# Kernel optimization log

Hardware: AMD Instinct MI355X
Metric: run time of the kernel (lower is better)

## Reference

```python
import jax, jax.numpy as jnp
import numpy as np

DIM = 256      # encoding dimensionality
S = 16         # alphabet size (one Linear per symbol)
OUT = 10       # number of classes
DEPTH = 14     # levels of the complete binary tree
N = 2 ** DEPTH - 1  # 16383 nodes, BFS layout (root = node 0)


def setup_inputs() -> dict:
    key = jax.random.key(0)
    k1, k2, k3, k4, k5 = jax.random.split(key, 5)
    # symbols per node
    x_sym = jax.random.randint(k1, (N,), 0, S, dtype=jnp.int32)
    # complete binary tree in BFS order: children of i are 2i+1, 2i+2; -1 = no child (leaf)
    idx = np.arange(N)
    child_idx = np.stack([2 * idx + 1, 2 * idx + 2], axis=1)
    child_idx[child_idx >= N] = -1
    child_idx = jnp.asarray(child_idx, dtype=jnp.int32)
    # per-symbol Linear(dim, dim) weights/biases, out Linear(dim, OUT)
    sc = 1.0 / np.sqrt(DIM)
    W = jax.random.normal(k2, (S, DIM, DIM), dtype=jnp.float32) * sc
    b = jax.random.normal(k3, (S, DIM), dtype=jnp.float32) * sc
    W_out = jax.random.normal(k4, (DIM, OUT), dtype=jnp.float32) * sc
    b_out = jax.random.normal(k5, (OUT,), dtype=jnp.float32) * sc
    return {"x_sym": x_sym, "child_idx": child_idx, "W": W, "b": b,
            "W_out": W_out, "b_out": b_out}


def reference(x_sym, child_idx, W, b, W_out, b_out):
    """Depth-batched, vectorized equivalent of the serial tree traversal.

    For each node i (children before parents):
      enc[i] = tanh(W[sym_i] @ mean(enc[children(i)]) + b[sym_i])
    Leaves use the zero vector as input (matching Linear(zeros) = bias).
    Output = enc[root] @ W_out + b_out.
    """
    n = x_sym.shape[0]
    depth = int(np.log2(n + 1))
    dim = W.shape[1]
    enc = jnp.zeros((n, dim), dtype=W.dtype)
    for d in range(depth - 1, -1, -1):  # deepest level first
        lo, hi = 2 ** d - 1, min(2 ** (d + 1) - 1, n)
        cidx = child_idx[lo:hi]                          # [m, 2]
        valid = (cidx >= 0)
        ch = enc[jnp.clip(cidx, 0)] * valid[..., None].astype(enc.dtype)  # [m,2,dim]
        cnt = valid.sum(-1, keepdims=True).astype(enc.dtype)
        mean = ch.sum(1) / jnp.maximum(cnt, 1.0)         # [m, dim]; zeros for leaves
        onehot = jax.nn.one_hot(x_sym[lo:hi], W.shape[0], dtype=enc.dtype)  # [m, S]
        pre = jnp.einsum('ns,nd,sde->ne', onehot, mean, W) + onehot @ b
        enc = enc.at[lo:hi].set(jnp.tanh(pre))
    return enc[0] @ W_out + b_out
```

## Files before the change

### kernel.cpp

```cpp
#include <hip/hip_runtime.h>

#define DIM 256
#define GRP 16
#define MPAD 260
#define NBLK 1024
#define CSTR 32

#define O11 0
#define O10 2288
#define O9  3552
#define OTOT 4352
#define G11_BLOCKS 572
#define G10_BLOCKS 316
#define G9_ITEMS   188

#define FMA4(a, sc, v) \
    a.x = fmaf((sc), (v).x, a.x); a.y = fmaf((sc), (v).y, a.y); \
    a.z = fmaf((sc), (v).z, a.z); a.w = fmaf((sc), (v).w, a.w);

__device__ __forceinline__ float ld1(const float* p) {
    union { unsigned int u; float f; } cv;
    cv.u = __hip_atomic_load((const unsigned int*)p, __ATOMIC_RELAXED,
                             __HIP_MEMORY_SCOPE_AGENT);
    return cv.f;
}
__device__ __forceinline__ float2 ld2(const float* p) {
    union { unsigned long long u; float2 f; } cv;
    cv.u = __hip_atomic_load((const unsigned long long*)p, __ATOMIC_RELAXED,
                             __HIP_MEMORY_SCOPE_AGENT);
    return cv.f;
}
__device__ __forceinline__ void st1f(float* p, float x) {
    union { unsigned int u; float f; } cv; cv.f = x;
    __hip_atomic_store((unsigned int*)p, cv.u, __ATOMIC_RELAXED,
                       __HIP_MEMORY_SCOPE_AGENT);
}
__device__ __forceinline__ void st2(float* p, float x, float y) {
    union { unsigned long long u; float2 f; } cv;
    cv.f = make_float2(x, y);
    __hip_atomic_store((unsigned long long*)p, cv.u, __ATOMIC_RELAXED,
                       __HIP_MEMORY_SCOPE_AGENT);
}
__device__ __forceinline__ int addi(int* p) {
    return __hip_atomic_fetch_add(p, 1, __ATOMIC_RELAXED, __HIP_MEMORY_SCOPE_AGENT);
}
__device__ __forceinline__ void spin4(const int* f) {
    if (__hip_atomic_load(f, __ATOMIC_RELAXED, __HIP_MEMORY_SCOPE_AGENT) >= 4) return;
    int guard = 0;
    do {
        __builtin_amdgcn_s_sleep(1);
        if (++guard > (1 << 20)) break;
    } while (__hip_atomic_load(f, __ATOMIC_RELAXED, __HIP_MEMORY_SCOPE_AGENT) < 4);
}

__device__ __forceinline__ void gemm_core(const float* __restrict__ Ws,
                                          const float mean_s[GRP][MPAD],
                                          float4 part_s[4][4][64],
                                          int w, int lane) {
    const int ns4 = (lane >> 4) << 2;
    float4 acc0 = make_float4(0, 0, 0, 0), acc1 = acc0, acc2 = acc0, acc3 = acc0;
    const int dbase = w * 64;
    #pragma unroll 4
    for (int dd = 0; dd < 64; dd += 4) {
        const float4 w0 = *(const float4*)(Ws + (size_t)(dd + 0) * DIM);
        const float4 w1 = *(const float4*)(Ws + (size_t)(dd + 1) * DIM);
        const float4 w2 = *(const float4*)(Ws + (size_t)(dd + 2) * DIM);
        const float4 w3 = *(const float4*)(Ws + (size_t)(dd + 3) * DIM);
        const int dk = dbase + dd;
        const float4 m0 = *(const float4*)(&mean_s[ns4 + 0][dk]);
        const float4 m1 = *(const float4*)(&mean_s[ns4 + 1][dk]);
        const float4 m2 = *(const float4*)(&mean_s[ns4 + 2][dk]);
        const float4 m3 = *(const float4*)(&mean_s[ns4 + 3][dk]);
        FMA4(acc0, m0.x, w0); FMA4(acc0, m0.y, w1); FMA4(acc0, m0.z, w2); FMA4(acc0, m0.w, w3);
        FMA4(acc1, m1.x, w0); FMA4(acc1, m1.y, w1); FMA4(acc1, m1.z, w2); FMA4(acc1, m1.w, w3);
        FMA4(acc2, m2.x, w0); FMA4(acc2, m2.y, w1); FMA4(acc2, m2.z, w2); FMA4(acc2, m2.w, w3);
        FMA4(acc3, m3.x, w0); FMA4(acc3, m3.y, w1); FMA4(acc3, m3.z, w2); FMA4(acc3, m3.w, w3);
    }
    part_s[w][0][lane] = acc0;
    part_s[w][1][lane] = acc1;
    part_s[w][2][lane] = acc2;
    part_s[w][3][lane] = acc3;
}

__device__ __forceinline__ void unpair(int p, int& pa, int& pb) {
    int a = 0, rem = p;
    while (rem >= 16 - a) { rem -= 16 - a; ++a; }
    pa = a; pb = a + rem;
}

__global__ __launch_bounds__(256) void combo_sort_zero(const int* __restrict__ x_sym,
                                                       const float* __restrict__ W,
                                                       const float* __restrict__ b,
                                                       float* __restrict__ T,
                                                       int* __restrict__ order,
                                                       int* __restrict__ cnt) {
    __shared__ float  mean_s[GRP][MPAD];
    __shared__ float4 part_s[4][4][64];
    __shared__ int cnt_s[16], cur_s[16];
    const int t = threadIdx.x;
    const int w = t >> 6;
    const int lane = t & 63;
    const int bid = blockIdx.x;

    if (bid < 576) {
        const int s = bid / 36;
        const int rem = bid % 36;
        const int chunk = rem >> 2;
        const int tile = rem & 3;
        {
            const int c = lane << 2;
            #pragma unroll
            for (int j = 0; j < 4; ++j) {
                const int p = chunk * 16 + w * 4 + j;
                float4 m = make_float4(0.f, 0.f, 0.f, 0.f);
                if (p < 136) {
                    int pa, pb; unpair(p, pa, pb);
                    const float4 ba = *(const float4*)(b + pa * DIM + c);
                    const float4 bb = *(const float4*)(b + pb * DIM + c);
                    m.x = 0.5f * (tanhf(ba.x) + tanhf(bb.x));
                    m.y = 0.5f * (tanhf(ba.y) + tanhf(bb.y));
                    m.z = 0.5f * (tanhf(ba.z) + tanhf(bb.z));
                    m.w = 0.5f * (tanhf(ba.w) + tanhf(bb.w));
                }
                *(float4*)(&mean_s[w * 4 + j][c]) = m;
            }
        }
        __syncthreads();
        const int ns4 = (lane >> 4) << 2;
        const int g4  = (lane & 15) << 2;
        gemm_core(W + ((size_t)s << 16) + (size_t)(w * 64) * DIM + tile * 64 + g4,
                  mean_s, part_s, w, lane);
        __syncthreads();
        const int p = chunk * 16 + ns4 + w;
        if (p < 136) {
            int pa, pb; unpair(p, pa, pb);
            float4 r        = part_s[0][w][lane];
            const float4 p1 = part_s[1][w][lane];
            const float4 p2 = part_s[2][w][lane];
            const float4 p3 = part_s[3][w][lane];
            const float4 bs = *(const float4*)(b + s * DIM + tile * 64 + g4);
            r.x = tanhf(r.x + p1.x + p2.x + p3.x + bs.x);
            r.y = tanhf(r.y + p1.y + p2.y + p3.y + bs.y);
            r.z = tanhf(r.z + p1.z + p2.z + p3.z + bs.z);
            r.w = tanhf(r.w + p1.w + p2.w + p3.w + bs.w);
            *(float4*)(T + (size_t)((s * 16 + pa) * 16 + pb) * DIM + tile * 64 + g4) = r;
            if (pa != pb)
                *(float4*)(T + (size_t)((s * 16 + pb) * 16 + pa) * DIM + tile * 64 + g4) = r;
        }
    } else if (bid <= 578) {
        const int li = bid - 576;
        const int d = 11 - li;
        const int off = (li == 0) ? O11 : (li == 1) ? O10 : O9;
        const int lo = (1 << d) - 1;
        const int n = 1 << d;
        for (int i = t; i < n + 240; i += 256) order[off + i] = -1;
        if (t < 16) cnt_s[t] = 0;
        __syncthreads();
        for (int i = t; i < n; i += 256) atomicAdd(&cnt_s[x_sym[lo + i]], 1);
        __syncthreads();
        if (t == 0) {
            int run = off;
            for (int s2 = 0; s2 < 16; ++s2) {
                cur_s[s2] = run;
                run += ((cnt_s[s2] + GRP - 1) / GRP) * GRP;
            }
        }
        __syncthreads();
        for (int i = t; i < n; i += 256) {
            const int pos = atomicAdd(&cur_s[x_sym[lo + i]], 1);
            order[pos] = lo + i;
        }
    } else {
        for (int i = t; i < 1024 * CSTR; i += 256) cnt[i] = 0;
    }
}

__global__ __launch_bounds__(256) void grouped_T(const int* __restrict__ x_sym,
                                                 const float* __restrict__ W,
                                                 const float* __restrict__ b,
                                                 float* __restrict__ enc,
                                                 const float* __restrict__ T,
                                                 const int* __restrict__ order) {
    const int base = (blockIdx.x >> 2) * GRP + O11;
    const int tile = blockIdx.x & 3;
    const int n0 = order[base];
    if (n0 < 0) return;
    const int s = x_sym[n0];
    const int t = threadIdx.x;
    const int w = t >> 6;
    const int lane = t & 63;
    __shared__ float  mean_s[GRP][MPAD];
    __shared__ float4 part_s[4][4][64];
    {
        const int c = lane << 2;
        #pragma unroll
        for (int j = 0; j < 4; ++j) {
            const int node = order[base + w * 4 + j];
            float4 m = make_float4(0.f, 0.f, 0.f, 0.f);
            if (node >= 0) {
                const int c0 = 2 * node + 1, c1 = c0 + 1;
                const float* r0 = T + (size_t)((x_sym[c0] * 16 + x_sym[2 * c0 + 1]) * 16
                                               + x_sym[2 * c0 + 2]) * DIM;
                const float* r1 = T + (size_t)((x_sym[c1] * 16 + x_sym[2 * c1 + 1]) * 16
                                               + x_sym[2 * c1 + 2]) * DIM;
                const float4 ea = *(const float4*)(r0 + c);
                const float4 eb = *(const float4*)(r1 + c);
                m.x = 0.5f * (ea.x + eb.x);
                m.y = 0.5f * (ea.y + eb.y);
                m.z = 0.5f * (ea.z + eb.z);
                m.w = 0.5f * (ea.w + eb.w);
            }
            *(float4*)(&mean_s[w * 4 + j][c]) = m;
        }
    }
    __syncthreads();
    const int ns4 = (lane >> 4) << 2;
    const int g4  = (lane & 15) << 2;
    gemm_core(W + ((size_t)s << 16) + (size_t)(w * 64) * DIM + tile * 64 + g4,
              mean_s, part_s, w, lane);
    __syncthreads();
    const int node_g = order[base + ns4 + w];
    if (node_g >= 0) {
        float4 r        = part_s[0][w][lane];
        const float4 p1 = part_s[1][w][lane];
        const float4 p2 = part_s[2][w][lane];
        const float4 p3 = part_s[3][w][lane];
        const float4 bs = *(const float4*)(b + s * DIM + tile * 64 + g4);
        r.x = tanhf(r.x + p1.x + p2.x + p3.x + bs.x);
        r.y = tanhf(r.y + p1.y + p2.y + p3.y + bs.y);
        r.z = tanhf(r.z + p1.z + p2.z + p3.z + bs.z);
        r.w = tanhf(r.w + p1.w + p2.w + p3.w + bs.w);
        *(float4*)(enc + (size_t)node_g * DIM + tile * 64 + g4) = r;
    }
}

__global__ __launch_bounds__(256) void grouped_enc(const int* __restrict__ x_sym,
                                                   const float* __restrict__ W,
                                                   const float* __restrict__ b,
                                                   float* __restrict__ enc,
                                                   const int* __restrict__ order,
                                                   int level_off) {
    const int base = (blockIdx.x >> 2) * GRP + level_off;
    const int tile = blockIdx.x & 3;
    const int n0 = order[base];
    if (n0 < 0) return;
    const int s = x_sym[n0];
    const int t = threadIdx.x;
    const int w = t >> 6;
    const int lane = t & 63;
    __shared__ float  mean_s[GRP][MPAD];
    __shared__ float4 part_s[4][4][64];
    {
        const int c = lane << 2;
        #pragma unroll
        for (int j = 0; j < 4; ++j) {
            const int node = order[base + w * 4 + j];
            float4 m = make_float4(0.f, 0.f, 0.f, 0.f);
            if (node >= 0) {
                const int c0 = 2 * node + 1;
                const float4 ea = *(const float4*)(enc + (size_t)c0 * DIM + c);
                const float4 eb = *(const float4*)(enc + (size_t)(c0 + 1) * DIM + c);
                m.x = 0.5f * (ea.x + eb.x);
                m.y = 0.5f * (ea.y + eb.y);
                m.z = 0.5f * (ea.z + eb.z);
                m.w = 0.5f * (ea.w + eb.w);
            }
            *(float4*)(&mean_s[w * 4 + j][c]) = m;
        }
    }
    __syncthreads();
    const int ns4 = (lane >> 4) << 2;
    const int g4  = (lane & 15) << 2;
    gemm_core(W + ((size_t)s << 16) + (size_t)(w * 64) * DIM + tile * 64 + g4,
              mean_s, part_s, w, lane);
    __syncthreads();
    const int node_g = order[base + ns4 + w];
    if (node_g >= 0) {
        float4 r        = part_s[0][w][lane];
        const float4 p1 = part_s[1][w][lane];
        const float4 p2 = part_s[2][w][lane];
        const float4 p3 = part_s[3][w][lane];
        const float4 bs = *(const float4*)(b + s * DIM + tile * 64 + g4);
        r.x = tanhf(r.x + p1.x + p2.x + p3.x + bs.x);
        r.y = tanhf(r.y + p1.y + p2.y + p3.y + bs.y);
        r.z = tanhf(r.z + p1.z + p2.z + p3.z + bs.z);
        r.w = tanhf(r.w + p1.w + p2.w + p3.w + bs.w);
        *(float4*)(enc + (size_t)node_g * DIM + tile * 64 + g4) = r;
    }
}

__global__ __launch_bounds__(256, 4) void tail_kernel(const int* __restrict__ x_sym,
                                                      const float* __restrict__ W,
                                                      const float* __restrict__ b,
                                                      float* __restrict__ enc,
                                                      const int* __restrict__ order,
                                                      int* __restrict__ cnt,
                                                      const float* __restrict__ W_out,
                                                      const float* __restrict__ b_out,
                                                      float* __restrict__ out) {
    __shared__ float  mean_s[GRP][MPAD];
    __shared__ float4 part_s[4][4][64];
    const int t = threadIdx.x;
    const int w = t >> 6;
    const int lane = t & 63;
    const int bid = blockIdx.x;

    if (bid < G9_ITEMS) {
        const int base = (bid >> 2) * GRP + O9;
        const int tile = bid & 3;
        const int n0 = order[base];
        if (n0 >= 0) {
            const int s = x_sym[n0];
            const int c = lane << 2;
            #pragma unroll
            for (int j = 0; j < 4; ++j) {
                const int node = order[base + w * 4 + j];
                float4 m = make_float4(0.f, 0.f, 0.f, 0.f);
                if (node >= 0) {
                    const int c0 = 2 * node + 1;
                    const float4 ea = *(const float4*)(enc + (size_t)c0 * DIM + c);
                    const float4 eb = *(const float4*)(enc + (size_t)(c0 + 1) * DIM + c);
                    m.x = 0.5f * (ea.x + eb.x);
                    m.y = 0.5f * (ea.y + eb.y);
                    m.z = 0.5f * (ea.z + eb.z);
                    m.w = 0.5f * (ea.w + eb.w);
                }
                *(float4*)(&mean_s[w * 4 + j][c]) = m;
            }
            __syncthreads();
            const int ns4 = (lane >> 4) << 2;
            const int g4  = (lane & 15) << 2;
            gemm_core(W + ((size_t)s << 16) + (size_t)(w * 64) * DIM + tile * 64 + g4,
                      mean_s, part_s, w, lane);
            __syncthreads();
            const int node_g = order[base + ns4 + w];
            if (node_g >= 0) {
                float4 r        = part_s[0][w][lane];
                const float4 p1 = part_s[1][w][lane];
                const float4 p2 = part_s[2][w][lane];
                const float4 p3 = part_s[3][w][lane];
                const float4 bs = *(const float4*)(b + s * DIM + tile * 64 + g4);
                r.x = tanhf(r.x + p1.x + p2.x + p3.x + bs.x);
                r.y = tanhf(r.y + p1.y + p2.y + p3.y + bs.y);
                r.z = tanhf(r.z + p1.z + p2.z + p3.z + bs.z);
                r.w = tanhf(r.w + p1.w + p2.w + p3.w + bs.w);
                float* ep = enc + (size_t)node_g * DIM + tile * 64 + g4;
                st2(ep, r.x, r.y);
                st2(ep + 2, r.z, r.w);
            }
            __syncthreads();
            if (t < 16) {
                const int ng = order[base + t];
                if (ng >= 0) addi(&cnt[ng * CSTR]);
            }
        }
        __syncthreads();
    }

    float* smean = (float*)&mean_s[0][0];
    float* spart = (float*)&part_s[0][0][0];
    for (int d = 8; d >= 0; --d) {
        const int items = 4 << d;
        if (bid >= items) return;
        const int node = (1 << d) - 1 + (bid >> 2);
        const int tile = bid & 3;
        const int c0 = 2 * node + 1;
        const int cc = tile * 64 + lane;
        const int s = x_sym[node];

        const float* Wp = W + ((size_t)s << 16) + (size_t)(w * 64) * DIM + cc;
        float wreg[64];
        #pragma unroll
        for (int i = 0; i < 64; ++i) wreg[i] = Wp[(size_t)i * DIM];
        #pragma unroll
        for (int i = 0; i < 64; ++i) asm volatile("" : "+v"(wreg[i]) :: "memory");

        if (t < 2) spin4(&cnt[(c0 + t) * CSTR]);
        __syncthreads();

        if (t < 128) {
            const int o = t << 1;
            const float2 a = ld2(enc + (size_t)c0 * DIM + o);
            const float2 bb = ld2(enc + (size_t)(c0 + 1) * DIM + o);
            *(float2*)&smean[o] = make_float2(0.5f * (a.x + bb.x), 0.5f * (a.y + bb.y));
        }
        __syncthreads();

        float acc0 = 0.0f, acc1 = 0.0f;
        const float* sm = smean + w * 64;
        #pragma unroll
        for (int i = 0; i < 64; i += 2) {
            acc0 = fmaf(sm[i], wreg[i], acc0);
            acc1 = fmaf(sm[i + 1], wreg[i + 1], acc1);
        }
        spart[t] = acc0 + acc1;
        __syncthreads();
        if (t < 64) {
            float r = spart[t] + spart[t + 64] + spart[t + 128] + spart[t + 192];
            r += b[s * DIM + tile * 64 + t];
            st1f(enc + (size_t)node * DIM + tile * 64 + t, tanhf(r));
        }
        __syncthreads();
        if (t == 0) addi(&cnt[node * CSTR]);
        __syncthreads();
    }

    if (bid == 0) {
        if (t == 0) spin4(&cnt[0]);
        __syncthreads();
        const float e = ld1(enc + t);
        float p[10];
        #pragma unroll
        for (int o = 0; o < 10; ++o) p[o] = e * W_out[t * 10 + o];
        #pragma unroll
        for (int o = 0; o < 10; ++o)
            #pragma unroll
            for (int k = 32; k >= 1; k >>= 1) p[o] += __shfl_xor(p[o], k, 64);
        float* hp = (float*)&part_s[0][0][0];
        if (lane == 0) {
            #pragma unroll
            for (int o = 0; o < 10; ++o) hp[w * 10 + o] = p[o];
        }
        __syncthreads();
        if (t < 10) out[t] = b_out[t] + hp[t] + hp[10 + t] + hp[20 + t] + hp[30 + t];
    }
}

__global__ __launch_bounds__(256) void level_small(const int* __restrict__ x_sym,
                                                   const float* __restrict__ W,
                                                   const float* __restrict__ b,
                                                   float* __restrict__ enc,
                                                   int lo, int N) {
    const int node = lo + (blockIdx.x >> 2);
    const int tile = blockIdx.x & 3;
    const int t = threadIdx.x;
    const int lane = t & 63;
    const int c = tile * 64 + lane;
    __shared__ float mean_s[DIM];
    __shared__ float part[256];
    const int s = x_sym[node];
    const int c0 = 2 * node + 1;
    float m = 0.0f;
    if (c0 < N)
        m = 0.5f * (enc[(size_t)c0 * DIM + t] + enc[(size_t)(c0 + 1) * DIM + t]);
    mean_s[t] = m;
    __syncthreads();
    float acc = 0.0f;
    if (c0 < N) {
        const float* __restrict__ Ws = W + ((size_t)s << 16);
        const int d0 = (t >> 6) * 64;
        #pragma unroll 8
        for (int d = d0; d < d0 + 64; ++d)
            acc = fmaf(mean_s[d], Ws[d * DIM + c], acc);
    }
    part[t] = acc;
    __syncthreads();
    if (t < 64) {
        float r = part[t] + part[t + 64] + part[t + 128] + part[t + 192];
        r += b[s * DIM + c];
        enc[(size_t)node * DIM + c] = tanhf(r);
    }
}

__global__ __launch_bounds__(256) void level_big(const int* __restrict__ x_sym,
                                                 const float* __restrict__ W,
                                                 const float* __restrict__ b,
                                                 float* __restrict__ enc,
                                                 int lo, int N) {
    const int node = lo + blockIdx.x;
    const int e = threadIdx.x;
    __shared__ float mean_s[DIM];
    const int s = x_sym[node];
    const int c0 = 2 * node + 1;
    float acc = b[s * DIM + e];
    if (c0 < N) {
        mean_s[e] = 0.5f * (enc[(size_t)c0 * DIM + e] + enc[(size_t)(c0 + 1) * DIM + e]);
        __syncthreads();
        const float* __restrict__ Ws = W + ((size_t)s << 16);
        #pragma unroll 8
        for (int d = 0; d < DIM; ++d)
            acc = fmaf(mean_s[d], Ws[d * DIM + e], acc);
    }
    enc[(size_t)node * DIM + e] = tanhf(acc);
}

__global__ void out_kernel(const float* __restrict__ enc,
                           const float* __restrict__ W_out,
                           const float* __restrict__ b_out,
                           float* __restrict__ out, int outn) {
    const int o = threadIdx.x;
    if (o < outn) {
        float acc = b_out[o];
        for (int d = 0; d < DIM; ++d)
            acc = fmaf(enc[d], W_out[d * outn + o], acc);
        out[o] = acc;
    }
}

extern "C" void kernel_launch(void* const* d_in, const int* in_sizes, int n_in,
                              void* d_out, int out_size, void* d_ws, size_t ws_size,
                              hipStream_t stream) {
    const int*   x_sym = (const int*)d_in[0];
    const float* W     = (const float*)d_in[2];
    const float* b     = (const float*)d_in[3];
    const float* W_out = (const float*)d_in[4];
    const float* b_out = (const float*)d_in[5];
    float* out = (float*)d_out;
    float* enc = (float*)d_ws;
    const int N = in_sizes[0];

    int depth = 0;
    while (((1 << depth) - 1) < N) ++depth;

    const size_t need = (size_t)16383 * DIM * 4 + (OTOT + 1024 * CSTR) * 4;
    if (N == (1 << 14) - 1 && out_size == 10 && ws_size >= need) {
        float* T   = enc + (size_t)8191 * DIM;
        int* order = (int*)(enc + (size_t)N * DIM);
        int* cnt   = order + OTOT;

        combo_sort_zero<<<580, 256, 0, stream>>>(x_sym, W, b, T, order, cnt);
        grouped_T<<<G11_BLOCKS, 256, 0, stream>>>(x_sym, W, b, enc, T, order);
        grouped_enc<<<G10_BLOCKS, 256, 0, stream>>>(x_sym, W, b, enc, order, O10);
        tail_kernel<<<NBLK, 256, 0, stream>>>(x_sym, W, b, enc, order, cnt,
                                              W_out, b_out, out);
    } else {
        for (int d = depth - 1; d >= 0; --d) {
            int lo = (1 << d) - 1;
            int n = (1 << d);
            if (lo + n > N) n = N - lo;
            if (n >= 256)
                level_big<<<n, 256, 0, stream>>>(x_sym, W, b, enc, lo, N);
            else
                level_small<<<n * 4, 256, 0, stream>>>(x_sym, W, b, enc, lo, N);
        }
        out_kernel<<<1, 64, 0, stream>>>(enc, W_out, b_out, out, out_size);
    }
}
```

Before: 67.06 us.

## Process two tree levels per block in tail to halve cross-block handoffs

Levels 8 down to 0 of the tail kernel previously split each node over four blocks, one per 64-column tile, and synchronised through flag counters at every level. Now one block computes a whole parent node together with its two child nodes, full 256 columns, reading the four grandchildren directly. The intent is to cut the number of spin-wait handoffs and launch-wide serial steps roughly in half. In exchange each block does more serial FMA work per column and loses the preloaded register weights, so per-level latency rises while parallelism across blocks drops.

```diff
diff --git a/kernel.cpp b/kernel.cpp
--- a/kernel.cpp
+++ b/kernel.cpp
@@ -44,13 +44,13 @@
 __device__ __forceinline__ int addi(int* p) {
     return __hip_atomic_fetch_add(p, 1, __ATOMIC_RELAXED, __HIP_MEMORY_SCOPE_AGENT);
 }
-__device__ __forceinline__ void spin4(const int* f) {
-    if (__hip_atomic_load(f, __ATOMIC_RELAXED, __HIP_MEMORY_SCOPE_AGENT) >= 4) return;
+__device__ __forceinline__ void spinN(const int* f, int thr) {
+    if (__hip_atomic_load(f, __ATOMIC_RELAXED, __HIP_MEMORY_SCOPE_AGENT) >= thr) return;
     int guard = 0;
     do {
         __builtin_amdgcn_s_sleep(1);
         if (++guard > (1 << 20)) break;
-    } while (__hip_atomic_load(f, __ATOMIC_RELAXED, __HIP_MEMORY_SCOPE_AGENT) < 4);
+    } while (__hip_atomic_load(f, __ATOMIC_RELAXED, __HIP_MEMORY_SCOPE_AGENT) < thr);
 }
 
 __device__ __forceinline__ void gemm_core(const float* __restrict__ Ws,
@@ -86,6 +86,20 @@
     int a = 0, rem = p;
     while (rem >= 16 - a) { rem -= 16 - a; ++a; }
     pa = a; pb = a + rem;
+}
+
+__device__ __forceinline__ float colvec(const float* __restrict__ Wcol,
+                                        const float* __restrict__ mb) {
+    float a0 = 0.f, a1 = 0.f, a2 = 0.f, a3 = 0.f;
+    #pragma unroll 8
+    for (int k = 0; k < 256; k += 4) {
+        const float4 m4 = *(const float4*)(mb + k);
+        a0 = fmaf(m4.x, Wcol[(size_t)(k + 0) * DIM], a0);
+        a1 = fmaf(m4.y, Wcol[(size_t)(k + 1) * DIM], a1);
+        a2 = fmaf(m4.z, Wcol[(size_t)(k + 2) * DIM], a2);
+        a3 = fmaf(m4.w, Wcol[(size_t)(k + 3) * DIM], a3);
+    }
+    return (a0 + a1) + (a2 + a3);
 }
 
 __global__ __launch_bounds__(256) void combo_sort_zero(const int* __restrict__ x_sym,
@@ -289,6 +303,42 @@
     }
 }
 
+__device__ __forceinline__ void stage_pair(int n, int thr, const int* __restrict__ x_sym,
+                                           const float* __restrict__ W,
+                                           const float* __restrict__ b,
+                                           float* __restrict__ enc, int* __restrict__ cnt,
+                                           float* G, float* E, float* MB, int t) {
+    const int g0 = 4 * n + 3;
+    if (t < 4) spinN(&cnt[(g0 + t) * CSTR], thr);
+    __syncthreads();
+    #pragma unroll
+    for (int i = 0; i < 2; ++i) {
+        const int slot = t + 256 * i;
+        const int r = slot >> 7;
+        const int j = (slot & 127) << 1;
+        const float2 v = ld2(enc + (size_t)(g0 + r) * DIM + j);
+        G[r * 256 + j] = v.x;
+        G[r * 256 + j + 1] = v.y;
+    }
+    __syncthreads();
+    #pragma unroll
+    for (int i = 0; i < 2; ++i) {
+        const int sc = x_sym[2 * n + 1 + i];
+        MB[t] = 0.5f * (G[(2 * i) * 256 + t] + G[(2 * i + 1) * 256 + t]);
+        __syncthreads();
+        E[i * 256 + t] = tanhf(colvec(W + ((size_t)sc << 16) + t, MB) + b[sc * DIM + t]);
+        __syncthreads();
+    }
+    const int sp = x_sym[n];
+    MB[t] = 0.5f * (E[t] + E[256 + t]);
+    __syncthreads();
+    const float pv = tanhf(colvec(W + ((size_t)sp << 16) + t, MB) + b[sp * DIM + t]);
+    st1f(enc + (size_t)n * DIM + t, pv);
+    __syncthreads();
+    if (t == 0) addi(&cnt[n * CSTR]);
+    __syncthreads();
+}
+
 __global__ __launch_bounds__(256, 4) void tail_kernel(const int* __restrict__ x_sym,
                                                       const float* __restrict__ W,
                                                       const float* __restrict__ b,
@@ -357,73 +407,40 @@
         __syncthreads();
     }
 
-    float* smean = (float*)&mean_s[0][0];
-    float* spart = (float*)&part_s[0][0][0];
-    for (int d = 8; d >= 0; --d) {
-        const int items = 4 << d;
-        if (bid >= items) return;
-        const int node = (1 << d) - 1 + (bid >> 2);
-        const int tile = bid & 3;
-        const int c0 = 2 * node + 1;
-        const int cc = tile * 64 + lane;
-        const int s = x_sym[node];
-
-        const float* Wp = W + ((size_t)s << 16) + (size_t)(w * 64) * DIM + cc;
-        float wreg[64];
+    if (bid >= 128) return;
+    float* G  = (float*)&mean_s[0][0];
+    float* E  = G + 4 * 256;
+    float* MB = E + 2 * 256;
+
+    stage_pair(127 + bid, 4, x_sym, W, b, enc, cnt, G, E, MB, t);
+    if (bid >= 32) return;
+    stage_pair(31 + bid, 1, x_sym, W, b, enc, cnt, G, E, MB, t);
+    if (bid >= 8) return;
+    stage_pair(7 + bid, 1, x_sym, W, b, enc, cnt, G, E, MB, t);
+    if (bid >= 2) return;
+    stage_pair(1 + bid, 1, x_sym, W, b, enc, cnt, G, E, MB, t);
+    if (bid >= 1) return;
+
+    if (t < 2) spinN(&cnt[(1 + t) * CSTR], 1);
+    __syncthreads();
+    MB[t] = 0.5f * (ld1(enc + DIM + t) + ld1(enc + 2 * DIM + t));
+    __syncthreads();
+    const int s0 = x_sym[0];
+    const float e = tanhf(colvec(W + ((size_t)s0 << 16) + t, MB) + b[s0 * DIM + t]);
+    float p[10];
+    #pragma unroll
+    for (int o = 0; o < 10; ++o) p[o] = e * W_out[t * 10 + o];
+    #pragma unroll
+    for (int o = 0; o < 10; ++o)
         #pragma unroll
-        for (int i = 0; i < 64; ++i) wreg[i] = Wp[(size_t)i * DIM];
+        for (int k = 32; k >= 1; k >>= 1) p[o] += __shfl_xor(p[o], k, 64);
+    float* hp = (float*)&part_s[0][0][0];
+    if ((t & 63) == 0) {
         #pragma unroll
-        for (int i = 0; i < 64; ++i) asm volatile("" : "+v"(wreg[i]) :: "memory");
-
-        if (t < 2) spin4(&cnt[(c0 + t) * CSTR]);
-        __syncthreads();
-
-        if (t < 128) {
-            const int o = t << 1;
-            const float2 a = ld2(enc + (size_t)c0 * DIM + o);
-            const float2 bb = ld2(enc + (size_t)(c0 + 1) * DIM + o);
-            *(float2*)&smean[o] = make_float2(0.5f * (a.x + bb.x), 0.5f * (a.y + bb.y));
-        }
-        __syncthreads();
-
-        float acc0 = 0.0f, acc1 = 0.0f;
-        const float* sm = smean + w * 64;
-        #pragma unroll
-        for (int i = 0; i < 64; i += 2) {
-            acc0 = fmaf(sm[i], wreg[i], acc0);
-            acc1 = fmaf(sm[i + 1], wreg[i + 1], acc1);
-        }
-        spart[t] = acc0 + acc1;
-        __syncthreads();
-        if (t < 64) {
-            float r = spart[t] + spart[t + 64] + spart[t + 128] + spart[t + 192];
-            r += b[s * DIM + tile * 64 + t];
-            st1f(enc + (size_t)node * DIM + tile * 64 + t, tanhf(r));
-        }
-        __syncthreads();
-        if (t == 0) addi(&cnt[node * CSTR]);
-        __syncthreads();
-    }
-
-    if (bid == 0) {
-        if (t == 0) spin4(&cnt[0]);
-        __syncthreads();
-        const float e = ld1(enc + t);
-        float p[10];
-        #pragma unroll
-        for (int o = 0; o < 10; ++o) p[o] = e * W_out[t * 10 + o];
-        #pragma unroll
-        for (int o = 0; o < 10; ++o)
-            #pragma unroll
-            for (int k = 32; k >= 1; k >>= 1) p[o] += __shfl_xor(p[o], k, 64);
-        float* hp = (float*)&part_s[0][0][0];
-        if (lane == 0) {
-            #pragma unroll
-            for (int o = 0; o < 10; ++o) hp[w * 10 + o] = p[o];
-        }
-        __syncthreads();
-        if (t < 10) out[t] = b_out[t] + hp[t] + hp[10 + t] + hp[20 + t] + hp[30 + t];
-    }
+        for (int o = 0; o < 10; ++o) hp[w * 10 + o] = p[o];
+    }
+    __syncthreads();
+    if (t < 10) out[t] = b_out[t] + hp[t] + hp[10 + t] + hp[20 + t] + hp[30 + t];
 }
 
 __global__ __launch_bounds__(256) void level_small(const int* __restrict__ x_sym,
```

Measured after the change: 97.17 us. 44.9% more time.

## Fuse level-11 and level-10 grouped kernels into persistent dataflow mega kernel

Applied to the files above, without the earlier changes.

Merges the separate grouped_T and grouped_enc launches into the existing tail kernel, so levels 11, 10 and 9 run as phases of one launch. Cross-level dependencies use per-node completion counters with spin-waits instead of kernel boundaries, and the counter array grows to cover more nodes, with the zeroing split over more blocks. This removes two launch gaps and lets later levels start as soon as their children are ready. In exchange it adds spin-wait latency and atomic loads and stores, and it depends on all waited-on blocks being resident at once, which risks deadlock or the timeout guard firing if they are not.

```diff
diff --git a/kernel.cpp b/kernel.cpp
--- a/kernel.cpp
+++ b/kernel.cpp
@@ -5,6 +5,7 @@
 #define MPAD 260
 #define NBLK 1024
 #define CSTR 32
+#define NCNT 4096
 
 #define O11 0
 #define O10 2288
@@ -44,13 +45,13 @@
 __device__ __forceinline__ int addi(int* p) {
     return __hip_atomic_fetch_add(p, 1, __ATOMIC_RELAXED, __HIP_MEMORY_SCOPE_AGENT);
 }
-__device__ __forceinline__ void spin4(const int* f) {
-    if (__hip_atomic_load(f, __ATOMIC_RELAXED, __HIP_MEMORY_SCOPE_AGENT) >= 4) return;
+__device__ __forceinline__ void spinN(const int* f, int thr) {
+    if (__hip_atomic_load(f, __ATOMIC_RELAXED, __HIP_MEMORY_SCOPE_AGENT) >= thr) return;
     int guard = 0;
     do {
         __builtin_amdgcn_s_sleep(1);
         if (++guard > (1 << 20)) break;
-    } while (__hip_atomic_load(f, __ATOMIC_RELAXED, __HIP_MEMORY_SCOPE_AGENT) < 4);
+    } while (__hip_atomic_load(f, __ATOMIC_RELAXED, __HIP_MEMORY_SCOPE_AGENT) < thr);
 }
 
 __device__ __forceinline__ void gemm_core(const float* __restrict__ Ws,
@@ -171,26 +172,36 @@
             order[pos] = lo + i;
         }
     } else {
-        for (int i = t; i < 1024 * CSTR; i += 256) cnt[i] = 0;
-    }
-}
-
-__global__ __launch_bounds__(256) void grouped_T(const int* __restrict__ x_sym,
-                                                 const float* __restrict__ W,
-                                                 const float* __restrict__ b,
-                                                 float* __restrict__ enc,
-                                                 const float* __restrict__ T,
-                                                 const int* __restrict__ order) {
-    const int base = (blockIdx.x >> 2) * GRP + O11;
-    const int tile = blockIdx.x & 3;
+        const int seg = (bid - 579) * (NCNT * CSTR / 4);
+        for (int i = t; i < NCNT * CSTR / 4; i += 256) cnt[seg + i] = 0;
+    }
+}
+
+template <int SRC>
+__device__ __forceinline__ void grouped_phase(const int* __restrict__ x_sym,
+                                              const float* __restrict__ W,
+                                              const float* __restrict__ b,
+                                              float* __restrict__ enc,
+                                              const float* __restrict__ T,
+                                              const int* __restrict__ order,
+                                              int* __restrict__ cnt,
+                                              int base, int tile,
+                                              float mean_s[GRP][MPAD],
+                                              float4 part_s[4][4][64],
+                                              int t, int w, int lane) {
     const int n0 = order[base];
     if (n0 < 0) return;
     const int s = x_sym[n0];
-    const int t = threadIdx.x;
-    const int w = t >> 6;
-    const int lane = t & 63;
-    __shared__ float  mean_s[GRP][MPAD];
-    __shared__ float4 part_s[4][4][64];
+    const int ns4 = (lane >> 4) << 2;
+    const int g4  = (lane & 15) << 2;
+
+    if (SRC == 1) {
+        if (t < 32) {
+            const int pn = order[base + (t >> 1)];
+            if (pn >= 0) spinN(&cnt[(2 * pn + 1 + (t & 1)) * CSTR], 4);
+        }
+        __syncthreads();
+    }
     {
         const int c = lane << 2;
         #pragma unroll
@@ -199,23 +210,32 @@
             float4 m = make_float4(0.f, 0.f, 0.f, 0.f);
             if (node >= 0) {
                 const int c0 = 2 * node + 1, c1 = c0 + 1;
-                const float* r0 = T + (size_t)((x_sym[c0] * 16 + x_sym[2 * c0 + 1]) * 16
-                                               + x_sym[2 * c0 + 2]) * DIM;
-                const float* r1 = T + (size_t)((x_sym[c1] * 16 + x_sym[2 * c1 + 1]) * 16
-                                               + x_sym[2 * c1 + 2]) * DIM;
-                const float4 ea = *(const float4*)(r0 + c);
-                const float4 eb = *(const float4*)(r1 + c);
-                m.x = 0.5f * (ea.x + eb.x);
-                m.y = 0.5f * (ea.y + eb.y);
-                m.z = 0.5f * (ea.z + eb.z);
-                m.w = 0.5f * (ea.w + eb.w);
+                if (SRC == 0) {
+                    const float* r0 = T + (size_t)((x_sym[c0] * 16 + x_sym[2 * c0 + 1]) * 16
+                                                   + x_sym[2 * c0 + 2]) * DIM;
+                    const float* r1 = T + (size_t)((x_sym[c1] * 16 + x_sym[2 * c1 + 1]) * 16
+                                                   + x_sym[2 * c1 + 2]) * DIM;
+                    const float4 ea = *(const float4*)(r0 + c);
+                    const float4 eb = *(const float4*)(r1 + c);
+                    m.x = 0.5f * (ea.x + eb.x);
+                    m.y = 0.5f * (ea.y + eb.y);
+                    m.z = 0.5f * (ea.z + eb.z);
+                    m.w = 0.5f * (ea.w + eb.w);
+                } else {
+                    const float2 a0 = ld2(enc + (size_t)c0 * DIM + c);
+                    const float2 a1 = ld2(enc + (size_t)c0 * DIM + c + 2);
+                    const float2 b0 = ld2(enc + (size_t)c1 * DIM + c);
+                    const float2 b1 = ld2(enc + (size_t)c1 * DIM + c + 2);
+                    m.x = 0.5f * (a0.x + b0.x);
+                    m.y = 0.5f * (a0.y + b0.y);
+                    m.z = 0.5f * (a1.x + b1.x);
+                    m.w = 0.5f * (a1.y + b1.y);
+                }
             }
             *(float4*)(&mean_s[w * 4 + j][c]) = m;
         }
     }
     __syncthreads();
-    const int ns4 = (lane >> 4) << 2;
-    const int g4  = (lane & 15) << 2;
     gemm_core(W + ((size_t)s << 16) + (size_t)(w * 64) * DIM + tile * 64 + g4,
               mean_s, part_s, w, lane);
     __syncthreads();
@@ -230,69 +250,23 @@
         r.y = tanhf(r.y + p1.y + p2.y + p3.y + bs.y);
         r.z = tanhf(r.z + p1.z + p2.z + p3.z + bs.z);
         r.w = tanhf(r.w + p1.w + p2.w + p3.w + bs.w);
-        *(float4*)(enc + (size_t)node_g * DIM + tile * 64 + g4) = r;
-    }
-}
-
-__global__ __launch_bounds__(256) void grouped_enc(const int* __restrict__ x_sym,
-                                                   const float* __restrict__ W,
-                                                   const float* __restrict__ b,
-                                                   float* __restrict__ enc,
-                                                   const int* __restrict__ order,
-                                                   int level_off) {
-    const int base = (blockIdx.x >> 2) * GRP + level_off;
-    const int tile = blockIdx.x & 3;
-    const int n0 = order[base];
-    if (n0 < 0) return;
-    const int s = x_sym[n0];
-    const int t = threadIdx.x;
-    const int w = t >> 6;
-    const int lane = t & 63;
-    __shared__ float  mean_s[GRP][MPAD];
-    __shared__ float4 part_s[4][4][64];
-    {
-        const int c = lane << 2;
-        #pragma unroll
-        for (int j = 0; j < 4; ++j) {
-            const int node = order[base + w * 4 + j];
-            float4 m = make_float4(0.f, 0.f, 0.f, 0.f);
-            if (node >= 0) {
-                const int c0 = 2 * node + 1;
-                const float4 ea = *(const float4*)(enc + (size_t)c0 * DIM + c);
-                const float4 eb = *(const float4*)(enc + (size_t)(c0 + 1) * DIM + c);
-                m.x = 0.5f * (ea.x + eb.x);
-                m.y = 0.5f * (ea.y + eb.y);
-                m.z = 0.5f * (ea.z + eb.z);
-                m.w = 0.5f * (ea.w + eb.w);
-            }
-            *(float4*)(&mean_s[w * 4 + j][c]) = m;
-        }
-    }
-    __syncthreads();
-    const int ns4 = (lane >> 4) << 2;
-    const int g4  = (lane & 15) << 2;
-    gemm_core(W + ((size_t)s << 16) + (size_t)(w * 64) * DIM + tile * 64 + g4,
-              mean_s, part_s, w, lane);
-    __syncthreads();
-    const int node_g = order[base + ns4 + w];
-    if (node_g >= 0) {
-        float4 r        = part_s[0][w][lane];
-        const float4 p1 = part_s[1][w][lane];
-        const float4 p2 = part_s[2][w][lane];
-        const float4 p3 = part_s[3][w][lane];
-        const float4 bs = *(const float4*)(b + s * DIM + tile * 64 + g4);
-        r.x = tanhf(r.x + p1.x + p2.x + p3.x + bs.x);
-        r.y = tanhf(r.y + p1.y + p2.y + p3.y + bs.y);
-        r.z = tanhf(r.z + p1.z + p2.z + p3.z + bs.z);
-        r.w = tanhf(r.w + p1.w + p2.w + p3.w + bs.w);
-        *(float4*)(enc + (size_t)node_g * DIM + tile * 64 + g4) = r;
-    }
-}
-
-__global__ __launch_bounds__(256, 4) void tail_kernel(const int* __restrict__ x_sym,
+        float* ep = enc + (size_t)node_g * DIM + tile * 64 + g4;
+        st2(ep, r.x, r.y);
+        st2(ep + 2, r.z, r.w);
+    }
+    __syncthreads();
+    if (t < 16) {
+        const int ng = order[base + t];
+        if (ng >= 0) addi(&cnt[ng * CSTR]);
+    }
+    __syncthreads();
+}
+
+__global__ __launch_bounds__(256, 4) void mega_kernel(const int* __restrict__ x_sym,
                                                       const float* __restrict__ W,
                                                       const float* __restrict__ b,
                                                       float* __restrict__ enc,
+                                                      const float* __restrict__ T,
                                                       const int* __restrict__ order,
                                                       int* __restrict__ cnt,
                                                       const float* __restrict__ W_out,
@@ -305,57 +279,19 @@
     const int lane = t & 63;
     const int bid = blockIdx.x;
 
-    if (bid < G9_ITEMS) {
-        const int base = (bid >> 2) * GRP + O9;
-        const int tile = bid & 3;
-        const int n0 = order[base];
-        if (n0 >= 0) {
-            const int s = x_sym[n0];
-            const int c = lane << 2;
-            #pragma unroll
-            for (int j = 0; j < 4; ++j) {
-                const int node = order[base + w * 4 + j];
-                float4 m = make_float4(0.f, 0.f, 0.f, 0.f);
-                if (node >= 0) {
-                    const int c0 = 2 * node + 1;
-                    const float4 ea = *(const float4*)(enc + (size_t)c0 * DIM + c);
-                    const float4 eb = *(const float4*)(enc + (size_t)(c0 + 1) * DIM + c);
-                    m.x = 0.5f * (ea.x + eb.x);
-                    m.y = 0.5f * (ea.y + eb.y);
-                    m.z = 0.5f * (ea.z + eb.z);
-                    m.w = 0.5f * (ea.w + eb.w);
-                }
-                *(float4*)(&mean_s[w * 4 + j][c]) = m;
-            }
-            __syncthreads();
-            const int ns4 = (lane >> 4) << 2;
-            const int g4  = (lane & 15) << 2;
-            gemm_core(W + ((size_t)s << 16) + (size_t)(w * 64) * DIM + tile * 64 + g4,
-                      mean_s, part_s, w, lane);
-            __syncthreads();
-            const int node_g = order[base + ns4 + w];
-            if (node_g >= 0) {
-                float4 r        = part_s[0][w][lane];
-                const float4 p1 = part_s[1][w][lane];
-                const float4 p2 = part_s[2][w][lane];
-                const float4 p3 = part_s[3][w][lane];
-                const float4 bs = *(const float4*)(b + s * DIM + tile * 64 + g4);
-                r.x = tanhf(r.x + p1.x + p2.x + p3.x + bs.x);
-                r.y = tanhf(r.y + p1.y + p2.y + p3.y + bs.y);
-                r.z = tanhf(r.z + p1.z + p2.z + p3.z + bs.z);
-                r.w = tanhf(r.w + p1.w + p2.w + p3.w + bs.w);
-                float* ep = enc + (size_t)node_g * DIM + tile * 64 + g4;
-                st2(ep, r.x, r.y);
-                st2(ep + 2, r.z, r.w);
-            }
-            __syncthreads();
-            if (t < 16) {
-                const int ng = order[base + t];
-                if (ng >= 0) addi(&cnt[ng * CSTR]);
-            }
-        }
-        __syncthreads();
-    }
+    if (bid < G11_BLOCKS)
+        grouped_phase<0>(x_sym, W, b, enc, T, order, cnt,
+                         (bid >> 2) * GRP + O11, bid & 3, mean_s, part_s, t, w, lane);
+
+    if (bid >= G11_BLOCKS && bid < G11_BLOCKS + G10_BLOCKS) {
+        const int lb = bid - G11_BLOCKS;
+        grouped_phase<1>(x_sym, W, b, enc, T, order, cnt,
+                         (lb >> 2) * GRP + O10, lb & 3, mean_s, part_s, t, w, lane);
+    }
+
+    if (bid < G9_ITEMS)
+        grouped_phase<1>(x_sym, W, b, enc, T, order, cnt,
+                         (bid >> 2) * GRP + O9, bid & 3, mean_s, part_s, t, w, lane);
 
     float* smean = (float*)&mean_s[0][0];
     float* spart = (float*)&part_s[0][0][0];
@@ -375,7 +311,7 @@
         #pragma unroll
         for (int i = 0; i < 64; ++i) asm volatile("" : "+v"(wreg[i]) :: "memory");
 
-        if (t < 2) spin4(&cnt[(c0 + t) * CSTR]);
+        if (t < 2) spinN(&cnt[(c0 + t) * CSTR], 4);
         __syncthreads();
 
         if (t < 128) {
@@ -406,7 +342,7 @@
     }
 
     if (bid == 0) {
-        if (t == 0) spin4(&cnt[0]);
+        if (t == 0) spinN(&cnt[0], 4);
         __syncthreads();
         const float e = ld1(enc + t);
         float p[10];
@@ -512,16 +448,14 @@
     int depth = 0;
     while (((1 << depth) - 1) < N) ++depth;
 
-    const size_t need = (size_t)16383 * DIM * 4 + (OTOT + 1024 * CSTR) * 4;
+    const size_t need = (size_t)16383 * DIM * 4 + (OTOT + (size_t)NCNT * CSTR) * 4;
     if (N == (1 << 14) - 1 && out_size == 10 && ws_size >= need) {
         float* T   = enc + (size_t)8191 * DIM;
         int* order = (int*)(enc + (size_t)N * DIM);
         int* cnt   = order + OTOT;
 
-        combo_sort_zero<<<580, 256, 0, stream>>>(x_sym, W, b, T, order, cnt);
-        grouped_T<<<G11_BLOCKS, 256, 0, stream>>>(x_sym, W, b, enc, T, order);
-        grouped_enc<<<G10_BLOCKS, 256, 0, stream>>>(x_sym, W, b, enc, order, O10);
-        tail_kernel<<<NBLK, 256, 0, stream>>>(x_sym, W, b, enc, order, cnt,
+        combo_sort_zero<<<583, 256, 0, stream>>>(x_sym, W, b, T, order, cnt);
+        mega_kernel<<<NBLK, 256, 0, stream>>>(x_sym, W, b, enc, T, order, cnt,
                                               W_out, b_out, out);
     } else {
         for (int d = depth - 1; d >= 0; --d) {
```

After: 71.29 us. 1.06x slower.

## Split tail-level matvec into eight column tiles staged through LDS

Applied to the files above, without the earlier changes.

Tail levels 8..0 now split each node's 256-wide output into 8 tiles of 32 columns instead of 4 tiles of 64, doubling the blocks per level. Each block stages its W slice in padded LDS rather than holding 64 weights in registers, and uses an 8-way k-split reduction. The readiness thresholds on child counters change to 8, except level 8, whose children are still written by 4 tiles. Counter zeroing is spread across four blocks. The aim is more parallelism and lower register pressure on the latency-bound tail, at the cost of extra LDS traffic, an added barrier, and more atomic increments per node.

```diff
diff --git a/kernel.cpp b/kernel.cpp
--- a/kernel.cpp
+++ b/kernel.cpp
@@ -5,6 +5,7 @@
 #define MPAD 260
 #define NBLK 1024
 #define CSTR 32
+#define NCNT 1024
 
 #define O11 0
 #define O10 2288
@@ -44,13 +45,13 @@
 __device__ __forceinline__ int addi(int* p) {
     return __hip_atomic_fetch_add(p, 1, __ATOMIC_RELAXED, __HIP_MEMORY_SCOPE_AGENT);
 }
-__device__ __forceinline__ void spin4(const int* f) {
-    if (__hip_atomic_load(f, __ATOMIC_RELAXED, __HIP_MEMORY_SCOPE_AGENT) >= 4) return;
+__device__ __forceinline__ void spinN(const int* f, int thr) {
+    if (__hip_atomic_load(f, __ATOMIC_RELAXED, __HIP_MEMORY_SCOPE_AGENT) >= thr) return;
     int guard = 0;
     do {
         __builtin_amdgcn_s_sleep(1);
         if (++guard > (1 << 20)) break;
-    } while (__hip_atomic_load(f, __ATOMIC_RELAXED, __HIP_MEMORY_SCOPE_AGENT) < 4);
+    } while (__hip_atomic_load(f, __ATOMIC_RELAXED, __HIP_MEMORY_SCOPE_AGENT) < thr);
 }
 
 __device__ __forceinline__ void gemm_core(const float* __restrict__ Ws,
@@ -171,7 +172,8 @@
             order[pos] = lo + i;
         }
     } else {
-        for (int i = t; i < 1024 * CSTR; i += 256) cnt[i] = 0;
+        const int seg = (bid - 579) * (NCNT * CSTR / 4);
+        for (int i = t; i < NCNT * CSTR / 4; i += 256) cnt[seg + i] = 0;
     }
 }
 
@@ -298,8 +300,9 @@
                                                       const float* __restrict__ W_out,
                                                       const float* __restrict__ b_out,
                                                       float* __restrict__ out) {
-    __shared__ float  mean_s[GRP][MPAD];
-    __shared__ float4 part_s[4][4][64];
+    __shared__ float4 smem4[2240];
+    float (*mean_s)[MPAD] = (float(*)[MPAD])smem4;
+    float4 (*part_s)[4][64] = (float4(*)[4][64])((char*)smem4 + 16640);
     const int t = threadIdx.x;
     const int w = t >> 6;
     const int lane = t & 63;
@@ -357,56 +360,63 @@
         __syncthreads();
     }
 
-    float* smean = (float*)&mean_s[0][0];
-    float* spart = (float*)&part_s[0][0][0];
+    float* Wlds  = (float*)smem4;
+    float* smean = (float*)smem4 + 8448;
+    float* spart = (float*)smem4 + 8704;
+    const int col = t & 31;
+    const int kg  = t >> 5;
     for (int d = 8; d >= 0; --d) {
-        const int items = 4 << d;
+        const int items = 8 << d;
         if (bid >= items) return;
-        const int node = (1 << d) - 1 + (bid >> 2);
-        const int tile = bid & 3;
-        const int c0 = 2 * node + 1;
-        const int cc = tile * 64 + lane;
-        const int s = x_sym[node];
-
-        const float* Wp = W + ((size_t)s << 16) + (size_t)(w * 64) * DIM + cc;
-        float wreg[64];
-        #pragma unroll
-        for (int i = 0; i < 64; ++i) wreg[i] = Wp[(size_t)i * DIM];
-        #pragma unroll
-        for (int i = 0; i < 64; ++i) asm volatile("" : "+v"(wreg[i]) :: "memory");
-
-        if (t < 2) spin4(&cnt[(c0 + t) * CSTR]);
-        __syncthreads();
-
-        if (t < 128) {
-            const int o = t << 1;
-            const float2 a = ld2(enc + (size_t)c0 * DIM + o);
-            const float2 bb = ld2(enc + (size_t)(c0 + 1) * DIM + o);
-            *(float2*)&smean[o] = make_float2(0.5f * (a.x + bb.x), 0.5f * (a.y + bb.y));
-        }
-        __syncthreads();
-
-        float acc0 = 0.0f, acc1 = 0.0f;
-        const float* sm = smean + w * 64;
-        #pragma unroll
-        for (int i = 0; i < 64; i += 2) {
-            acc0 = fmaf(sm[i], wreg[i], acc0);
-            acc1 = fmaf(sm[i + 1], wreg[i + 1], acc1);
-        }
-        spart[t] = acc0 + acc1;
-        __syncthreads();
-        if (t < 64) {
-            float r = spart[t] + spart[t + 64] + spart[t + 128] + spart[t + 192];
-            r += b[s * DIM + tile * 64 + t];
-            st1f(enc + (size_t)node * DIM + tile * 64 + t, tanhf(r));
-        }
-        __syncthreads();
-        if (t == 0) addi(&cnt[node * CSTR]);
-        __syncthreads();
+        const int thr = (d == 8) ? 4 : 8;
+        for (int it = bid; it < items; it += NBLK) {
+            const int node = (1 << d) - 1 + (it >> 3);
+            const int tile = it & 7;
+            const int c0 = 2 * node + 1;
+            const int s = x_sym[node];
+
+            const float* Wp = W + ((size_t)s << 16) + tile * 32 + col;
+            #pragma unroll
+            for (int i = 0; i < 32; ++i) {
+                const int k = kg + (i << 3);
+                Wlds[k * 33 + col] = Wp[(size_t)k * DIM];
+            }
+            __syncthreads();
+
+            if (t < 2) spinN(&cnt[(c0 + t) * CSTR], thr);
+            __syncthreads();
+
+            if (t < 128) {
+                const int o = t << 1;
+                const float2 a  = ld2(enc + (size_t)c0 * DIM + o);
+                const float2 bb = ld2(enc + (size_t)(c0 + 1) * DIM + o);
+                *(float2*)&smean[o] = make_float2(0.5f * (a.x + bb.x),
+                                                  0.5f * (a.y + bb.y));
+            }
+            __syncthreads();
+
+            float acc = 0.0f;
+            const int k0 = kg << 5;
+            #pragma unroll
+            for (int kk = 0; kk < 32; ++kk)
+                acc = fmaf(smean[k0 + kk], Wlds[(k0 + kk) * 33 + col], acc);
+            spart[t] = acc;
+            __syncthreads();
+            if (t < 32) {
+                float r = 0.0f;
+                #pragma unroll
+                for (int kc = 0; kc < 8; ++kc) r += spart[kc * 32 + t];
+                r += b[s * DIM + tile * 32 + t];
+                st1f(enc + (size_t)node * DIM + tile * 32 + t, tanhf(r));
+            }
+            __syncthreads();
+            if (t == 0) addi(&cnt[node * CSTR]);
+            __syncthreads();
+        }
     }
 
     if (bid == 0) {
-        if (t == 0) spin4(&cnt[0]);
+        if (t == 0) spinN(&cnt[0], 8);
         __syncthreads();
         const float e = ld1(enc + t);
         float p[10];
@@ -416,7 +426,7 @@
         for (int o = 0; o < 10; ++o)
             #pragma unroll
             for (int k = 32; k >= 1; k >>= 1) p[o] += __shfl_xor(p[o], k, 64);
-        float* hp = (float*)&part_s[0][0][0];
+        float* hp = (float*)smem4;
         if (lane == 0) {
             #pragma unroll
             for (int o = 0; o < 10; ++o) hp[w * 10 + o] = p[o];
@@ -512,13 +522,13 @@
     int depth = 0;
     while (((1 << depth) - 1) < N) ++depth;
 
-    const size_t need = (size_t)16383 * DIM * 4 + (OTOT + 1024 * CSTR) * 4;
+    const size_t need = (size_t)16383 * DIM * 4 + (OTOT + (size_t)NCNT * CSTR) * 4;
     if (N == (1 << 14) - 1 && out_size == 10 && ws_size >= need) {
         float* T   = enc + (size_t)8191 * DIM;
         int* order = (int*)(enc + (size_t)N * DIM);
         int* cnt   = order + OTOT;
 
-        combo_sort_zero<<<580, 256, 0, stream>>>(x_sym, W, b, T, order, cnt);
+        combo_sort_zero<<<583, 256, 0, stream>>>(x_sym, W, b, T, order, cnt);
         grouped_T<<<G11_BLOCKS, 256, 0, stream>>>(x_sym, W, b, enc, T, order);
         grouped_enc<<<G10_BLOCKS, 256, 0, stream>>>(x_sym, W, b, enc, order, O10);
         tail_kernel<<<NBLK, 256, 0, stream>>>(x_sym, W, b, enc, order, cnt,
```

Result: slower. 72.99 us (+8.8%).
